# Performance work log

Hardware: AMD Instinct MI355X
Metric: run time of the kernel (lower is better)

Reference implementation:

```python
import jax, jax.numpy as jnp
import numpy as np

B, L, C = 2048, 2048, 16
F = L // 2                 # num_freqs = 1024
H = 4 * F                  # multi_factor * num_freqs = 4096
P = int(len(np.unique(L // np.arange(1, F + 1))))  # n patch sizes = 88
SCALE = 0.02
NOISE_EPS = 0.01


def setup_inputs() -> dict:
    key = jax.random.key(0)
    ks = jax.random.split(key, 10)
    return {
        "x": jax.random.normal(ks[0], (B, L, C), jnp.float32),
        "w_start": SCALE * jax.random.normal(ks[1], (C, 1), jnp.float32),
        "b_start": SCALE * jax.random.normal(ks[2], (1,), jnp.float32),
        "w1": SCALE * jax.random.normal(ks[3], (2, F, H), jnp.float32),
        "b1": SCALE * jax.random.normal(ks[4], (2, H), jnp.float32),
        "w2": SCALE * jax.random.normal(ks[5], (2, H, F), jnp.float32),
        "b2": SCALE * jax.random.normal(ks[6], (2, F), jnp.float32),
        "w_gate": SCALE * jax.random.normal(ks[7], (F, P), jnp.float32),
        "w_noise": SCALE * jax.random.normal(ks[8], (F, P), jnp.float32),
        "noise_z": jax.random.normal(ks[9], (B, P), jnp.float32),
        "top_k": 3,
    }


def reference(x, w_start, b_start, w1, b1, w2, b2, w_gate, w_noise, noise_z, top_k):
    # start_fc: [B, L, C] -> [B, L, 1] -> [B, 1, L]
    v = (jnp.einsum("blc,co->blo", x, w_start) + b_start).transpose(0, 2, 1)
    # rfft (ortho), drop DC bin -> [B, 1, F] complex
    xf = jnp.fft.rfft(v, axis=-1, norm="ortho")[:, :, 1:]
    xr, xi = jnp.real(xf), jnp.imag(xf)
    # complex 2-layer MLP in frequency domain
    o1r = jax.nn.relu(jnp.einsum("bdi,io->bdo", xr, w1[0]) - jnp.einsum("bdi,io->bdo", xi, w1[1]) + b1[0])
    o1i = jax.nn.relu(jnp.einsum("bdi,io->bdo", xi, w1[0]) + jnp.einsum("bdi,io->bdo", xr, w1[1]) + b1[1])
    o2r = jnp.einsum("bdo,of->bdf", o1r, w2[0]) - jnp.einsum("bdo,of->bdf", o1i, w2[1]) + b2[0]
    o2i = jnp.einsum("bdo,of->bdf", o1i, w2[0]) + jnp.einsum("bdo,of->bdf", o1r, w2[1]) + b2[1]
    amp = jnp.sqrt(o2r * o2r + o2i * o2i)[:, 0, :]  # [B, F]
    # router logits with (training) noise injection
    clean_logits = amp @ w_gate                      # [B, P]
    noise_std = jax.nn.softplus(amp @ w_noise) + NOISE_EPS
    logits = clean_logits + noise_z * noise_std
    # top-k -> softmax over top-k -> scatter into sparse gates
    top_w, top_i = jax.lax.top_k(logits, top_k)
    top_w = jax.nn.softmax(top_w, axis=-1)
    rows = jnp.arange(logits.shape[0])[:, None]
    gates = jnp.zeros_like(logits).at[rows, top_i].set(top_w)
    return gates
```

## Files before the change

### kernel.cpp

```cpp
#include <hip/hip_runtime.h>
#include <hip/hip_bf16.h>
#include <math.h>

#define B_DIM 2048
#define L_DIM 2048
#define F_DIM 1024
#define H_DIM 4096
#define P_DIM 88

typedef unsigned short u16;
typedef short bf16x8 __attribute__((ext_vector_type(8)));
typedef float f32x4 __attribute__((ext_vector_type(4)));

__device__ __forceinline__ u16 f2bf(float x) {
    unsigned u = __float_as_uint(x);
    return (u16)((u + 0x7fffu + ((u >> 16) & 1u)) >> 16);
}
__device__ __forceinline__ float bf2f(u16 h) {
    return __uint_as_float(((unsigned)h) << 16);
}

__device__ __forceinline__ void gload_lds16(const void* g, void* l) {
    unsigned loff = (unsigned)(uintptr_t)l;
    __builtin_amdgcn_global_load_lds(
        reinterpret_cast<const __attribute__((address_space(1))) void*>(
            reinterpret_cast<uintptr_t>(g)),
        reinterpret_cast<__attribute__((address_space(3))) void*>(loff),
        16, 0, 0);
}

__global__ __launch_bounds__(256) void prep_kernel(
    const float* __restrict__ x, const float* __restrict__ w_start,
    const float* __restrict__ b_start, u16* __restrict__ A1,
    const float* __restrict__ w1, u16* __restrict__ BT1)
{
    __shared__ float re[2048];
    __shared__ float im[2048];
    __shared__ float twr[1024];
    __shared__ float twi[1024];
    __shared__ float t0s[32][33];
    __shared__ float t1s[32][33];

    const int tid = threadIdx.x;

    if (blockIdx.x < 1024) {
        int b = blockIdx.x;
        const size_t row0 = (size_t)(2 * b) * 2048;

        const float4* wp = (const float4*)w_start;
        float4 w0 = wp[0], w1v = wp[1], w2 = wp[2], w3 = wp[3];
        float bs = b_start[0];

        for (int i = tid; i < 1024; i += 256) {
            float ang = -6.283185307179586f * ((float)i / 2048.0f);
            sincosf(ang, &twi[i], &twr[i]);
        }

        for (int l = tid; l < 2048; l += 256) {
            const float4* xp0 = (const float4*)(x + (row0 + l) * 16);
            const float4* xp1 = (const float4*)(x + (row0 + 2048 + l) * 16);
            float4 a0 = xp0[0], a1 = xp0[1], a2 = xp0[2], a3 = xp0[3];
            float4 c0 = xp1[0], c1 = xp1[1], c2 = xp1[2], c3 = xp1[3];
            float va = bs, vb = bs;
            va += a0.x * w0.x + a0.y * w0.y + a0.z * w0.z + a0.w * w0.w;
            va += a1.x * w1v.x + a1.y * w1v.y + a1.z * w1v.z + a1.w * w1v.w;
            va += a2.x * w2.x + a2.y * w2.y + a2.z * w2.z + a2.w * w2.w;
            va += a3.x * w3.x + a3.y * w3.y + a3.z * w3.z + a3.w * w3.w;
            vb += c0.x * w0.x + c0.y * w0.y + c0.z * w0.z + c0.w * w0.w;
            vb += c1.x * w1v.x + c1.y * w1v.y + c1.z * w1v.z + c1.w * w1v.w;
            vb += c2.x * w2.x + c2.y * w2.y + c2.z * w2.z + c2.w * w2.w;
            vb += c3.x * w3.x + c3.y * w3.y + c3.z * w3.z + c3.w * w3.w;
            unsigned j = __brev((unsigned)l) >> 21;
            re[j] = va;
            im[j] = vb;
        }
        __syncthreads();

        for (int s = 1; s <= 11; s++) {
            int half = 1 << (s - 1);
            for (int t = tid; t < 1024; t += 256) {
                int j = t & (half - 1);
                int base = (t >> (s - 1)) << s;
                int idx = j << (11 - s);
                float wr = twr[idx], wi = twi[idx];
                int i0 = base + j, i1 = i0 + half;
                float br = re[i1], bi = im[i1];
                float tr = br * wr - bi * wi;
                float ti = br * wi + bi * wr;
                float ar = re[i0], ai = im[i0];
                re[i0] = ar + tr; im[i0] = ai + ti;
                re[i1] = ar - tr; im[i1] = ai - ti;
            }
            __syncthreads();
        }

        const float sc = 0.5f * 0.022097086912079612f;
        u16* r0 = A1 + (size_t)(2 * b) * 4096;
        u16* r1 = r0 + 4096;
        for (int t = tid; t < 1024; t += 256) {
            int k = t + 1;
            int nk = 2048 - k;
            float Zr = re[k], Zi = im[k], Yr = re[nk], Yi = im[nk];
            float Ar = (Zr + Yr) * sc;
            float Ai = (Zi - Yi) * sc;
            float Br = (Zi + Yi) * sc;
            float Bi = (Yr - Zr) * sc;
            u16 h, lo;
            h = f2bf(Ar); lo = f2bf(Ar - bf2f(h)); r0[t] = h; r0[1024 + t] = lo;
            h = f2bf(Ai); lo = f2bf(Ai - bf2f(h)); r0[2048 + t] = h; r0[3072 + t] = lo;
            h = f2bf(Br); lo = f2bf(Br - bf2f(h)); r1[t] = h; r1[1024 + t] = lo;
            h = f2bf(Bi); lo = f2bf(Bi - bf2f(h)); r1[2048 + t] = h; r1[3072 + t] = lo;
        }
    } else {
        const int Kc = F_DIM, Nh = H_DIM;
        int bid = blockIdx.x - 1024;
        int k0 = (bid & 31) * 32;
        int n0 = (bid >> 5) * 32;
        int tx = tid & 31, ty = tid >> 5;
        const float* w0 = w1;
        const float* w1b = w1 + (size_t)Kc * Nh;

#pragma unroll
        for (int i = 0; i < 4; i++) {
            int k = k0 + ty + 8 * i;
            t0s[ty + 8 * i][tx] = w0[(size_t)k * Nh + n0 + tx];
            t1s[ty + 8 * i][tx] = w1b[(size_t)k * Nh + n0 + tx];
        }
        __syncthreads();

        size_t K4 = 4 * (size_t)Kc;
        int k = k0 + tx;
#pragma unroll
        for (int i = 0; i < 4; i++) {
            int nl = ty + 8 * i;
            int n = n0 + nl;
            float br = t0s[tx][nl];
            float bi = t1s[tx][nl];
            u16 brh = f2bf(br); u16 brl = f2bf(br - bf2f(brh));
            float nbi = -bi;
            u16 nih = f2bf(nbi); u16 nil = f2bf(nbi - bf2f(nih));
            u16 pih = f2bf(bi);  u16 pil = f2bf(bi - bf2f(pih));
            u16* rowr = BT1 + (size_t)n * K4;
            rowr[0 * Kc + k] = brh; rowr[1 * Kc + k] = brl;
            rowr[2 * Kc + k] = nih; rowr[3 * Kc + k] = nil;
            u16* rowi = BT1 + (size_t)(Nh + n) * K4;
            rowi[0 * Kc + k] = pih; rowi[1 * Kc + k] = pil;
            rowi[2 * Kc + k] = brh; rowi[3 * Kc + k] = brl;
        }
    }
}

__global__ __launch_bounds__(256) void conv_bt_kernel(
    const float* __restrict__ w, u16* __restrict__ BT, int Kc, int Nh)
{
    __shared__ float t0[32][33];
    __shared__ float t1[32][33];
    int k0 = blockIdx.x * 32, n0 = blockIdx.y * 32;
    int tx = threadIdx.x, ty = threadIdx.y;
    const float* w0 = w;
    const float* w1 = w + (size_t)Kc * Nh;

#pragma unroll
    for (int i = 0; i < 4; i++) {
        int k = k0 + ty + 8 * i;
        t0[ty + 8 * i][tx] = w0[(size_t)k * Nh + n0 + tx];
        t1[ty + 8 * i][tx] = w1[(size_t)k * Nh + n0 + tx];
    }
    __syncthreads();

    size_t K4 = 4 * (size_t)Kc;
    int k = k0 + tx;
#pragma unroll
    for (int i = 0; i < 4; i++) {
        int nl = ty + 8 * i;
        int n = n0 + nl;
        float br = t0[tx][nl];
        float bi = t1[tx][nl];
        u16 brh = f2bf(br); u16 brl = f2bf(br - bf2f(brh));
        float nbi = -bi;
        u16 nih = f2bf(nbi); u16 nil = f2bf(nbi - bf2f(nih));
        u16 pih = f2bf(bi);  u16 pil = f2bf(bi - bf2f(pih));
        u16* rowr = BT + (size_t)n * K4;
        rowr[0 * Kc + k] = brh; rowr[1 * Kc + k] = brl;
        rowr[2 * Kc + k] = nih; rowr[3 * Kc + k] = nil;
        u16* rowi = BT + (size_t)(Nh + n) * K4;
        rowi[0 * Kc + k] = pih; rowi[1 * Kc + k] = pil;
        rowi[2 * Kc + k] = brh; rowi[3 * Kc + k] = brl;
    }
}

extern __shared__ char smem8p[];

template <int EPI, int SWZ>
__global__ __launch_bounds__(1024, 4) void gemm8p(
    const u16* __restrict__ A, const u16* __restrict__ B,
    const float* __restrict__ biasL, const float* __restrict__ biasR,
    u16* __restrict__ OutU, float* __restrict__ P01, float* __restrict__ P23,
    int Kc, int KcLog, int NH, int nt)
{
    char* ldsA = smem8p;
    char* ldsB = smem8p + 65536;

    const int tid = threadIdx.x;
    const int w = tid >> 6, lane = tid & 63;
    const int wr = w >> 2, wc = w & 3;
    const int fr = lane & 15, kb = lane >> 4;

    int bx, by, z;
    if (SWZ == 1) {
        int b = blockIdx.x;
        int xcd = b & 7, idx = b >> 3;
        bx = 4 * xcd + (idx & 3);
        by = idx >> 2;
        z = 0;
    } else if (SWZ == 2) {
        int b = blockIdx.x;
        by = b & 7;
        int s = b >> 3;
        bx = s & 7;
        z = s >> 3;
    } else {
        bx = blockIdx.x; by = blockIdx.y; z = blockIdx.z;
    }
    const int n0 = bx * 256, m0 = by * 256;
    const size_t K4 = 4 * (size_t)Kc;

    const int srow = tid >> 2;
    const int lk8 = (((tid & 3) ^ ((tid >> 3) & 3))) * 8;
    const int wb = w * 1024;

    const int laneOff = fr * 64 + ((kb ^ ((fr >> 1) & 3)) << 4);

    f32x4 acc[4][4];
#pragma unroll
    for (int i = 0; i < 4; i++)
#pragma unroll
        for (int j = 0; j < 4; j++)
            acc[i][j] = (f32x4){0.f, 0.f, 0.f, 0.f};

    const int t0 = z * nt, te = t0 + nt;

    auto colA = [&](int t) {
        int k0 = t << 5;
        int seg = k0 >> KcLog, kk = k0 & (Kc - 1);
        int r3 = seg >= 3 ? seg - 3 : seg;
        int bs = seg >= 3 ? 2 : 0;
        return (bs + (r3 == 1 ? 1 : 0)) * Kc + kk;
    };
    auto colB = [&](int t) {
        int k0 = t << 5;
        int seg = k0 >> KcLog, kk = k0 & (Kc - 1);
        int r3 = seg >= 3 ? seg - 3 : seg;
        int bs = seg >= 3 ? 2 : 0;
        return (bs + (r3 == 2 ? 1 : 0)) * Kc + kk;
    };
    auto stageA = [&](int t) {
        const u16* src = A + (size_t)(m0 + srow) * K4 + colA(t) + lk8;
        gload_lds16(src, ldsA + (t & 3) * 16384 + wb);
    };
    auto stageB = [&](int t) {
        const u16* src = B + (size_t)(n0 + srow) * K4 + colB(t) + lk8;
        gload_lds16(src, ldsB + (t & 3) * 16384 + wb);
    };
    auto aBase = [&](int t) -> const char* {
        return ldsA + (t & 3) * 16384 + wr * 4096 + laneOff;
    };
    auto bBase = [&](int t) -> const char* {
        return ldsB + (t & 3) * 16384 + wc * 4096 + laneOff;
    };

    stageA(t0); stageB(t0);
    if (t0 + 1 < te) {
        stageA(t0 + 1); stageB(t0 + 1);
        asm volatile("s_waitcnt vmcnt(2)" ::: "memory");
    } else {
        asm volatile("s_waitcnt vmcnt(0)" ::: "memory");
    }
    asm volatile("s_barrier" ::: "memory");

    bf16x8 a0, a1, b0, b1, b2, b3;
    {
        const char* aS = aBase(t0);
        const char* bS = bBase(t0);
        a0 = *(const bf16x8*)(aS + 0 * 1024);
        a1 = *(const bf16x8*)(aS + 1 * 1024);
        b0 = *(const bf16x8*)(bS + 0 * 1024);
        b1 = *(const bf16x8*)(bS + 1 * 1024);
        b2 = *(const bf16x8*)(bS + 2 * 1024);
        b3 = *(const bf16x8*)(bS + 3 * 1024);
    }

    for (int t = t0; t < te; ++t) {
        const bool haveStage = (t + 2 < te);
        const bool haveNext  = (t + 1 < te);

        if (haveStage) { stageA(t + 2); stageB(t + 2); }

        const char* aS = aBase(t);
        bf16x8 c0 = *(const bf16x8*)(aS + 2 * 1024);
        bf16x8 c1 = *(const bf16x8*)(aS + 3 * 1024);

        __builtin_amdgcn_s_setprio(1);
        acc[0][0] = __builtin_amdgcn_mfma_f32_16x16x32_bf16(a0, b0, acc[0][0], 0, 0, 0);
        acc[0][1] = __builtin_amdgcn_mfma_f32_16x16x32_bf16(a0, b1, acc[0][1], 0, 0, 0);
        acc[0][2] = __builtin_amdgcn_mfma_f32_16x16x32_bf16(a0, b2, acc[0][2], 0, 0, 0);
        acc[0][3] = __builtin_amdgcn_mfma_f32_16x16x32_bf16(a0, b3, acc[0][3], 0, 0, 0);
        acc[1][0] = __builtin_amdgcn_mfma_f32_16x16x32_bf16(a1, b0, acc[1][0], 0, 0, 0);
        acc[1][1] = __builtin_amdgcn_mfma_f32_16x16x32_bf16(a1, b1, acc[1][1], 0, 0, 0);
        acc[1][2] = __builtin_amdgcn_mfma_f32_16x16x32_bf16(a1, b2, acc[1][2], 0, 0, 0);
        acc[1][3] = __builtin_amdgcn_mfma_f32_16x16x32_bf16(a1, b3, acc[1][3], 0, 0, 0);
        __builtin_amdgcn_s_setprio(0);

        if (haveStage) asm volatile("s_waitcnt vmcnt(2)" ::: "memory");
        else           asm volatile("s_waitcnt vmcnt(0)" ::: "memory");
        asm volatile("s_barrier" ::: "memory");

        if (haveNext) {
            const char* aN = aBase(t + 1);
            a0 = *(const bf16x8*)(aN + 0 * 1024);
            a1 = *(const bf16x8*)(aN + 1 * 1024);
        }

        __builtin_amdgcn_s_setprio(1);
        acc[2][0] = __builtin_amdgcn_mfma_f32_16x16x32_bf16(c0, b0, acc[2][0], 0, 0, 0);
        acc[2][1] = __builtin_amdgcn_mfma_f32_16x16x32_bf16(c0, b1, acc[2][1], 0, 0, 0);
        acc[2][2] = __builtin_amdgcn_mfma_f32_16x16x32_bf16(c0, b2, acc[2][2], 0, 0, 0);
        acc[2][3] = __builtin_amdgcn_mfma_f32_16x16x32_bf16(c0, b3, acc[2][3], 0, 0, 0);
        acc[3][0] = __builtin_amdgcn_mfma_f32_16x16x32_bf16(c1, b0, acc[3][0], 0, 0, 0);
        acc[3][1] = __builtin_amdgcn_mfma_f32_16x16x32_bf16(c1, b1, acc[3][1], 0, 0, 0);
        acc[3][2] = __builtin_amdgcn_mfma_f32_16x16x32_bf16(c1, b2, acc[3][2], 0, 0, 0);
        acc[3][3] = __builtin_amdgcn_mfma_f32_16x16x32_bf16(c1, b3, acc[3][3], 0, 0, 0);
        __builtin_amdgcn_s_setprio(0);

        if (haveNext) {
            const char* bN = bBase(t + 1);
            b0 = *(const bf16x8*)(bN + 0 * 1024);
            b1 = *(const bf16x8*)(bN + 1 * 1024);
            b2 = *(const bf16x8*)(bN + 2 * 1024);
            b3 = *(const bf16x8*)(bN + 3 * 1024);
        }
    }

    const int fq = kb;
#pragma unroll
    for (int nj = 0; nj < 4; nj++) {
        int n = n0 + wc * 64 + nj * 16 + fr;
        if (EPI == 0) {
            bool left = (n < NH);
            int nn = left ? n : (n - NH);
            float bias = left ? biasL[n] : biasR[nn];
#pragma unroll
            for (int mi = 0; mi < 4; mi++) {
                int mb = m0 + wr * 64 + mi * 16 + fq * 4;
#pragma unroll
                for (int r = 0; r < 4; r++) {
                    float val = fmaxf(acc[mi][nj][r] + bias, 0.f);
                    u16 h = f2bf(val);
                    u16 lo = f2bf(val - bf2f(h));
                    size_t rb = (size_t)(mb + r) * (4 * (size_t)NH);
                    if (left) { OutU[rb + nn] = h; OutU[rb + NH + nn] = lo; }
                    else { OutU[rb + 2 * (size_t)NH + nn] = h; OutU[rb + 3 * (size_t)NH + nn] = lo; }
                }
            }
        } else {
            const size_t PSZ = (size_t)2048 * 2048;
            float* Out = (z < 2) ? (P01 + (size_t)z * PSZ) : (P23 + (size_t)(z - 2) * PSZ);
#pragma unroll
            for (int mi = 0; mi < 4; mi++) {
                int mb = m0 + wr * 64 + mi * 16 + fq * 4;
#pragma unroll
                for (int r = 0; r < 4; r++)
                    Out[(size_t)(mb + r) * 2048 + n] = acc[mi][nj][r];
            }
        }
    }
}

__global__ __launch_bounds__(256) void router_kernel(
    const float* __restrict__ P01, const float* __restrict__ P23, int ZK,
    const float* __restrict__ b2,
    const float* __restrict__ w_gate, const float* __restrict__ w_noise,
    const float* __restrict__ noise_z, float* __restrict__ gates)
{
    __shared__ float s_amp[8][1024];
    __shared__ float s_dot[8][176];
    __shared__ float s_lg[8][88];
    __shared__ int   s_idx[8][3];
    __shared__ float s_val[8][3];

    const int tid = threadIdx.x;
    const int r0 = blockIdx.x * 8;
    const size_t PSZ = (size_t)2048 * 2048;

    for (int idx = tid; idx < 8 * 1024; idx += 256) {
        int row = idx >> 10, i = idx & 1023;
        size_t roff = (size_t)(r0 + row) * 2048;
        float orr = b2[i];
        float oii = b2[1024 + i];
        for (int zz = 0; zz < ZK; zz++) {
            const float* Pz = ((zz < 2) ? (P01 + (size_t)zz * PSZ)
                                        : (P23 + (size_t)(zz - 2) * PSZ)) + roff;
            orr += Pz[i];
            oii += Pz[1024 + i];
        }
        s_amp[row][i] = sqrtf(orr * orr + oii * oii);
    }
    __syncthreads();

    for (int idx = tid; idx < 8 * 176; idx += 256) {
        int row = idx / 176, c = idx % 176;
        const float* wcol = (c < 88) ? (w_gate + c) : (w_noise + (c - 88));
        float s = 0.f;
        const float4* av = (const float4*)s_amp[row];
        for (int k4 = 0; k4 < 256; k4++) {
            float4 a = av[k4];
            int k = k4 * 4;
            s = fmaf(a.x, wcol[(size_t)(k + 0) * 88], s);
            s = fmaf(a.y, wcol[(size_t)(k + 1) * 88], s);
            s = fmaf(a.z, wcol[(size_t)(k + 2) * 88], s);
            s = fmaf(a.w, wcol[(size_t)(k + 3) * 88], s);
        }
        s_dot[row][c] = s;
    }
    __syncthreads();

    for (int idx = tid; idx < 8 * 88; idx += 256) {
        int row = idx / 88, c = idx % 88;
        float cn = s_dot[row][88 + c];
        float ns = (cn > 20.f) ? cn : log1pf(expf(cn));
        ns += 0.01f;
        s_lg[row][c] = s_dot[row][c] + noise_z[(size_t)(r0 + row) * 88 + c] * ns;
    }
    __syncthreads();

    if (tid < 8) {
        int i0 = -1, i1 = -1, i2 = -1;
        float v0 = -1e30f, v1 = -1e30f, v2 = -1e30f;
        for (int i = 0; i < P_DIM; i++) {
            float t = s_lg[tid][i];
            if (t > v0) { v0 = t; i0 = i; }
        }
        for (int i = 0; i < P_DIM; i++) {
            if (i == i0) continue;
            float t = s_lg[tid][i];
            if (t > v1) { v1 = t; i1 = i; }
        }
        for (int i = 0; i < P_DIM; i++) {
            if (i == i0 || i == i1) continue;
            float t = s_lg[tid][i];
            if (t > v2) { v2 = t; i2 = i; }
        }
        s_idx[tid][0] = i0; s_idx[tid][1] = i1; s_idx[tid][2] = i2;
        s_val[tid][0] = v0; s_val[tid][1] = v1; s_val[tid][2] = v2;
    }
    __syncthreads();

    for (int idx = tid; idx < 8 * 88; idx += 256) {
        int row = idx / 88, c = idx % 88;
        float m = s_val[row][0];
        float e0 = expf(s_val[row][0] - m);
        float e1 = expf(s_val[row][1] - m);
        float e2 = expf(s_val[row][2] - m);
        float inv = 1.f / (e0 + e1 + e2);
        float g = 0.f;
        if (c == s_idx[row][0]) g = e0 * inv;
        else if (c == s_idx[row][1]) g = e1 * inv;
        else if (c == s_idx[row][2]) g = e2 * inv;
        gates[(size_t)(r0 + row) * 88 + c] = g;
    }
}

extern "C" void kernel_launch(void* const* d_in, const int* in_sizes, int n_in,
                              void* d_out, int out_size, void* d_ws, size_t ws_size,
                              hipStream_t stream)
{
    const float* x       = (const float*)d_in[0];
    const float* w_start = (const float*)d_in[1];
    const float* b_start = (const float*)d_in[2];
    const float* w1      = (const float*)d_in[3];
    const float* b1      = (const float*)d_in[4];
    const float* w2      = (const float*)d_in[5];
    const float* b2      = (const float*)d_in[6];
    const float* w_gate  = (const float*)d_in[7];
    const float* w_noise = (const float*)d_in[8];
    const float* noise_z = (const float*)d_in[9];
    float* gates = (float*)d_out;

    const size_t MB = 1024 * 1024;
    char* base = (char*)d_ws;
    u16*  A1   = (u16*)(base + 16 * MB);
    u16*  BT   = (u16*)(base + 32 * MB);
    u16*  A2   = (u16*)(base + 96 * MB);
    float* P01 = (float*)base;
    float* P23 = (float*)(base + 160 * MB);

    int ZK = (ws_size >= (size_t)192 * MB) ? 4 : 2;

    hipFuncSetAttribute(reinterpret_cast<const void*>(&gemm8p<0, 1>),
                        hipFuncAttributeMaxDynamicSharedMemorySize, 131072);
    hipFuncSetAttribute(reinterpret_cast<const void*>(&gemm8p<1, 2>),
                        hipFuncAttributeMaxDynamicSharedMemorySize, 131072);

    prep_kernel<<<1024 + 4096, 256, 0, stream>>>(
        x, w_start, b_start, A1, w1, BT);

    gemm8p<0, 1><<<256, 1024, 131072, stream>>>(
        A1, BT, b1, b1 + H_DIM, A2, nullptr, nullptr, F_DIM, 10, H_DIM, 192);

    conv_bt_kernel<<<dim3(H_DIM / 32, F_DIM / 32), dim3(32, 8), 0, stream>>>(
        w2, BT, H_DIM, F_DIM);
    gemm8p<1, 2><<<64 * ZK, 1024, 131072, stream>>>(
        A2, BT, nullptr, nullptr, nullptr, P01, P23, H_DIM, 12, F_DIM, 768 / ZK);

    router_kernel<<<B_DIM / 8, 256, 0, stream>>>(
        P01, P23, ZK, b2, w_gate, w_noise, noise_z, gates);
}
```

Baseline: 585.3 us.

## Replace first GEMM with 8-wave quadrant-pipelined kernel using K=64 tiles

Adds a new gemm_q8 kernel for the first frequency-domain GEMM. It uses 512 threads with each wave owning a larger 128x64 accumulator tile, stages K=64 chunks double-buffered in LDS via direct global-to-LDS loads, and interleaves quarter-tile LDS reads and async staging with MFMA bursts under barriers and setprio. The aim is more data reuse per wave and better overlap of memory with MFMA, at the cost of higher register pressure and many barriers per iteration.

After: 629.0 us. +7.5%, slower.

```diff
diff --git a/kernel.cpp b/kernel.cpp
--- a/kernel.cpp
+++ b/kernel.cpp
@@ -191,6 +191,185 @@
 
 extern __shared__ char smem8p[];
 
+#define GQ_BAR  asm volatile("s_barrier" ::: "memory")
+#define GQ_LGKM asm volatile("s_waitcnt lgkmcnt(0)" ::: "memory"); \
+                __builtin_amdgcn_sched_barrier(0)
+
+#define GQ_MFMA(m, n)                                                          \
+    __builtin_amdgcn_s_setprio(1);                                             \
+    _Pragma("unroll") for (int mi = 0; mi < 4; mi++) {                         \
+        _Pragma("unroll") for (int nj = 0; nj < 2; nj++) {                     \
+            _Pragma("unroll") for (int kc = 0; kc < 2; kc++) {                 \
+                acc[(m)*4+mi][(n)*2+nj] =                                      \
+                    __builtin_amdgcn_mfma_f32_16x16x32_bf16(                   \
+                        af[mi][kc], bfr[nj][kc], acc[(m)*4+mi][(n)*2+nj],      \
+                        0, 0, 0);                                              \
+            }                                                                  \
+        }                                                                      \
+    }                                                                          \
+    __builtin_amdgcn_s_setprio(0);
+
+template <int SWZ>
+__global__ __launch_bounds__(512, 2) void gemm_q8(
+    const u16* __restrict__ A, const u16* __restrict__ B,
+    const float* __restrict__ biasL, const float* __restrict__ biasR,
+    u16* __restrict__ OutU, int Kc, int KcLog, int NH, int nt)
+{
+    const int tid = threadIdx.x;
+    const int w = tid >> 6, lane = tid & 63;
+    const int wr = w >> 2, wc = w & 3;
+    const int fr = lane & 15, kb = lane >> 4;
+
+    int bx, by;
+    if (SWZ == 1) {
+        int b = blockIdx.x;
+        int xcd = b & 7, idx = b >> 3;
+        bx = 4 * xcd + (idx & 3);
+        by = idx >> 2;
+    } else {
+        bx = blockIdx.x; by = blockIdx.y;
+    }
+    const int n0 = bx * 256, m0 = by * 256;
+    const size_t K4 = 4 * (size_t)Kc;
+
+    const int rr0 = tid >> 3;
+    const int ee  = (((tid & 7) * 16) ^ ((rr0 & 7) << 4)) >> 1;
+
+    const int pre = fr * 128 + (((kb << 4) ^ ((fr & 7) << 4)));
+
+    f32x4 acc[8][4];
+#pragma unroll
+    for (int i = 0; i < 8; i++)
+#pragma unroll
+        for (int j = 0; j < 4; j++)
+            acc[i][j] = (f32x4){0.f, 0.f, 0.f, 0.f};
+
+    const int te = nt;
+
+    auto colOf = [&](int t, int isB) {
+        int k0 = t << 6;
+        int seg = k0 >> KcLog, kk = k0 & (Kc - 1);
+        int r3 = seg >= 3 ? seg - 3 : seg;
+        int bs = seg >= 3 ? 2 : 0;
+        int m = isB ? (r3 == 2 ? 1 : 0) : (r3 == 1 ? 1 : 0);
+        return (bs + m) * Kc + kk;
+    };
+    auto stageH = [&](int isB, int t, int h) {
+        int col = colOf(t, isB);
+        const u16* base = isB ? (B + (size_t)(n0 + h * 128) * K4)
+                              : (A + (size_t)(m0 + h * 128) * K4);
+        const u16* s0p = base + (size_t)rr0 * K4 + col + ee;
+        const u16* s1p = base + (size_t)(rr0 + 64) * K4 + col + ee;
+        char* dd = smem8p + (t & 1) * 65536 + isB * 32768 + h * 16384 + w * 1024;
+        gload_lds16(s0p, dd);
+        gload_lds16(s1p, dd + 8192);
+    };
+
+    bf16x8 af[4][2];
+    bf16x8 bfr[2][2];
+
+    auto readA = [&](int d, int m) {
+#pragma unroll
+        for (int mi = 0; mi < 4; mi++)
+#pragma unroll
+            for (int kc = 0; kc < 2; kc++)
+                af[mi][kc] = *(const bf16x8*)(smem8p + d * 65536 + m * 16384 +
+                    (wr * 64 + mi * 16) * 128 + (pre ^ (kc << 6)));
+    };
+    auto readB = [&](int d, int n) {
+#pragma unroll
+        for (int nj = 0; nj < 2; nj++)
+#pragma unroll
+            for (int kc = 0; kc < 2; kc++)
+                bfr[nj][kc] = *(const bf16x8*)(smem8p + d * 65536 + 32768 +
+                    n * 16384 + (wc * 32 + nj * 16) * 128 + (pre ^ (kc << 6)));
+    };
+
+    stageH(0, 0, 0); stageH(1, 0, 0); stageH(0, 0, 1); stageH(1, 0, 1);
+    stageH(0, 1, 0); stageH(1, 1, 0); stageH(0, 1, 1); stageH(1, 1, 1);
+    asm volatile("s_waitcnt vmcnt(4)" ::: "memory");
+    GQ_BAR;
+
+    for (int T = 0; T < te; T += 2) {
+        const bool first = (T == 0);
+        const bool s2 = (T + 2 < te);
+        const int d0 = T & 1, d1 = d0 ^ 1;
+
+        readA(d0, 0); readB(d0, 0);
+        if (!first) stageH(0, T + 1, 1);
+        GQ_BAR; GQ_LGKM;
+        GQ_MFMA(0, 0)
+        GQ_BAR;
+        readB(d0, 1);
+        if (!first) stageH(1, T + 1, 0);
+        GQ_BAR; GQ_LGKM;
+        GQ_MFMA(0, 1)
+        GQ_BAR;
+        readA(d0, 1);
+        if (s2) stageH(0, T + 2, 0);
+        GQ_BAR; GQ_LGKM;
+        GQ_MFMA(1, 1)
+        GQ_BAR;
+        readB(d0, 0);
+        if (s2) { stageH(1, T + 2, 1);
+                  asm volatile("s_waitcnt vmcnt(4)" ::: "memory"); }
+        else    { asm volatile("s_waitcnt vmcnt(0)" ::: "memory"); }
+        GQ_BAR; GQ_LGKM;
+        GQ_MFMA(1, 0)
+        GQ_BAR;
+        readA(d1, 0); readB(d1, 0);
+        if (s2) stageH(0, T + 2, 1);
+        GQ_BAR; GQ_LGKM;
+        GQ_MFMA(0, 0)
+        GQ_BAR;
+        readB(d1, 1);
+        if (s2) stageH(1, T + 2, 0);
+        GQ_BAR; GQ_LGKM;
+        GQ_MFMA(0, 1)
+        GQ_BAR;
+        readA(d1, 1);
+        if (s2) stageH(0, T + 3, 0);
+        GQ_BAR; GQ_LGKM;
+        GQ_MFMA(1, 1)
+        GQ_BAR;
+        readB(d1, 0);
+        if (s2) { stageH(1, T + 3, 1);
+                  asm volatile("s_waitcnt vmcnt(4)" ::: "memory"); }
+        else    { asm volatile("s_waitcnt vmcnt(0)" ::: "memory"); }
+        GQ_BAR; GQ_LGKM;
+        GQ_MFMA(1, 0)
+        GQ_BAR;
+    }
+
+#pragma unroll
+    for (int n = 0; n < 2; n++) {
+#pragma unroll
+        for (int nj = 0; nj < 2; nj++) {
+            int nn0 = n0 + n * 128 + wc * 32 + nj * 16 + fr;
+            bool left = (nn0 < NH);
+            int nn = left ? nn0 : (nn0 - NH);
+            float bias = left ? biasL[nn0] : biasR[nn];
+#pragma unroll
+            for (int m = 0; m < 2; m++) {
+#pragma unroll
+                for (int mi = 0; mi < 4; mi++) {
+#pragma unroll
+                    for (int r = 0; r < 4; r++) {
+                        int mb = m0 + m * 128 + wr * 64 + mi * 16 + kb * 4 + r;
+                        float val = fmaxf(acc[m * 4 + mi][n * 2 + nj][r] + bias, 0.f);
+                        u16 h = f2bf(val);
+                        u16 lo = f2bf(val - bf2f(h));
+                        size_t rb = (size_t)mb * (4 * (size_t)NH);
+                        if (left) { OutU[rb + nn] = h; OutU[rb + NH + nn] = lo; }
+                        else { OutU[rb + 2 * (size_t)NH + nn] = h;
+                               OutU[rb + 3 * (size_t)NH + nn] = lo; }
+                    }
+                }
+            }
+        }
+    }
+}
+
 template <int EPI, int SWZ>
 __global__ __launch_bounds__(1024, 4) void gemm8p(
     const u16* __restrict__ A, const u16* __restrict__ B,
@@ -228,7 +407,6 @@
     const int srow = tid >> 2;
     const int lk8 = (((tid & 3) ^ ((tid >> 3) & 3))) * 8;
     const int wb = w * 1024;
-
     const int laneOff = fr * 64 + ((kb ^ ((fr >> 1) & 3)) << 4);
 
     f32x4 acc[4][4];
@@ -496,7 +674,7 @@
 
     int ZK = (ws_size >= (size_t)192 * MB) ? 4 : 2;
 
-    hipFuncSetAttribute(reinterpret_cast<const void*>(&gemm8p<0, 1>),
+    hipFuncSetAttribute(reinterpret_cast<const void*>(&gemm_q8<1>),
                         hipFuncAttributeMaxDynamicSharedMemorySize, 131072);
     hipFuncSetAttribute(reinterpret_cast<const void*>(&gemm8p<1, 2>),
                         hipFuncAttributeMaxDynamicSharedMemorySize, 131072);
@@ -504,8 +682,8 @@
     prep_kernel<<<1024 + 4096, 256, 0, stream>>>(
         x, w_start, b_start, A1, w1, BT);
 
-    gemm8p<0, 1><<<256, 1024, 131072, stream>>>(
-        A1, BT, b1, b1 + H_DIM, A2, nullptr, nullptr, F_DIM, 10, H_DIM, 192);
+    gemm_q8<1><<<256, 512, 131072, stream>>>(
+        A1, BT, b1, b1 + H_DIM, A2, F_DIM, 10, H_DIM, 96);
 
     conv_bt_kernel<<<dim3(H_DIM / 32, F_DIM / 32), dim3(32, 8), 0, stream>>>(
         w2, BT, H_DIM, F_DIM);
```
